# Performance work log

Measured on AMD Instinct MI355X. Metric: run time of the kernel, lower is better.

The kernel has to match this reference:

```python
import jax, jax.numpy as jnp
import numpy as np

B, N_AIM, N_DET, C = 4, 2048, 2048, 256  # inplanes=256, inter_channels=128


def _lin(x, w, b):
    # torch nn.Linear: y = x @ W^T + b, weight shape [out, in]
    return jnp.einsum('bnc,dc->bnd', x, w) + b


def setup_inputs() -> dict:
    key = jax.random.key(0)
    ks = jax.random.split(key, 16)
    s = 1.0 / np.sqrt(C)
    inp = {
        'detect': jax.random.normal(ks[0], (B, N_DET, C), jnp.float32),
        'aim': jax.random.normal(ks[1], (B, N_AIM, C), jnp.float32),
    }
    names = ['g', 'g2', 'theta', 'phi', 'W', 'Q']
    for i, nm in enumerate(names):
        inp[nm + '_w'] = jax.random.uniform(ks[2 + 2 * i], (C, C), jnp.float32, -s, s)
        inp[nm + '_b'] = jax.random.uniform(ks[3 + 2 * i], (C,), jnp.float32, -s, s)
    return inp


def reference(detect, aim, g_w, g_b, g2_w, g2_b, theta_w, theta_b, phi_w, phi_b, W_w, W_b, Q_w, Q_b):
    b, na, c = aim.shape
    nd = detect.shape[1]
    ic = c // 2  # inter_channels

    # view(B, ic, -1) on a contiguous [B, N, C] tensor -> row-major reshape to [B, ic, 2N]
    d_x = _lin(detect, g_w, g_b).reshape(b, ic, -1).transpose(0, 2, 1)      # (B, 2Nd, ic)
    a_x = _lin(aim, g2_w, g2_b).reshape(b, ic, -1).transpose(0, 2, 1)       # (B, 2Na, ic)
    theta_x = _lin(aim, theta_w, theta_b).reshape(b, ic, -1).transpose(0, 2, 1)  # (B, 2Na, ic)
    phi_x = _lin(detect, phi_w, phi_b).reshape(b, ic, -1)                   # (B, ic, 2Nd)

    f = jnp.matmul(theta_x, phi_x)                 # (B, 2Na, 2Nd)
    f_div_C = f / f.shape[-1]                      # scale by 2*Nd
    fi_div_C = jnp.swapaxes(f, 1, 2) / f.shape[-2] # (B, 2Nd, 2Na), scale by 2*Na

    non_aim = jnp.matmul(f_div_C, d_x)             # (B, 2Na, ic)
    non_aim = non_aim.transpose(0, 2, 1).reshape(b, na, c)
    non_aim = _lin(non_aim, W_w, W_b) + aim

    non_det = jnp.matmul(fi_div_C, a_x)            # (B, 2Nd, ic)
    non_det = non_det.transpose(0, 2, 1).reshape(b, nd, c)
    non_det = _lin(non_det, Q_w, Q_b) + detect

    return (non_det, non_aim)
```

## Files before the change

kernel.cpp:

```cpp
#include <hip/hip_runtime.h>


typedef __attribute__((ext_vector_type(4))) float  f32x4;
typedef __attribute__((ext_vector_type(8))) __bf16 bf16x8;
typedef __attribute__((ext_vector_type(8))) unsigned short u16x8;
typedef __attribute__((ext_vector_type(4))) unsigned short u16x4;

__device__ inline unsigned short f2bf(float f) {
    union { float f; unsigned u; } c; c.f = f;
    unsigned r = c.u + 0x7FFF + ((c.u >> 16) & 1);
    return (unsigned short)(r >> 16);
}
__device__ inline bf16x8 ldfrag(const unsigned short* p) {
    return __builtin_bit_cast(bf16x8, *(const u16x8*)p);
}

__global__ __launch_bounds__(256)
void prep_kernel(const float* __restrict__ g_w, const float* __restrict__ g2_w,
                 const float* __restrict__ th_w, const float* __restrict__ ph_w,
                 const float* __restrict__ W_w, const float* __restrict__ Q_w,
                 const float* __restrict__ aim, const float* __restrict__ detect,
                 unsigned short* __restrict__ dst)
{
    const int z = blockIdx.y;
    const float* src; size_t n4; unsigned short* o;
    if (z == 0)      { src = g_w;    n4 = 16384;  o = dst; }
    else if (z == 1) { src = g2_w;   n4 = 16384;  o = dst + 65536; }
    else if (z == 2) { src = th_w;   n4 = 16384;  o = dst + 2 * 65536; }
    else if (z == 3) { src = ph_w;   n4 = 16384;  o = dst + 3 * 65536; }
    else if (z == 4) { src = W_w;    n4 = 16384;  o = dst + 4 * 65536; }
    else if (z == 5) { src = Q_w;    n4 = 16384;  o = dst + 5 * 65536; }
    else if (z == 6) { src = aim;    n4 = 524288; o = dst + 6 * 65536; }
    else             { src = detect; n4 = 524288; o = dst + 6 * 65536 + 2097152; }
    const size_t stride = (size_t)gridDim.x * 256;
    for (size_t i = blockIdx.x * 256 + threadIdx.x; i < n4; i += stride) {
        float4 v = ((const float4*)src)[i];
        u16x4 p; p[0]=f2bf(v.x); p[1]=f2bf(v.y); p[2]=f2bf(v.z); p[3]=f2bf(v.w);
        ((u16x4*)o)[i] = p;
    }
}

__global__ __launch_bounds__(256)
void lin4_kernel(const unsigned short* __restrict__ Abf, const unsigned short* __restrict__ Dbf,
                 const unsigned short* __restrict__ Wb,
                 const float* __restrict__ b_g, const float* __restrict__ b_g2,
                 const float* __restrict__ b_th, const float* __restrict__ b_ph,
                 unsigned short* __restrict__ T,  unsigned short* __restrict__ Ga,
                 unsigned short* __restrict__ P,  unsigned short* __restrict__ Gd)
{
    const int z = blockIdx.z, set = blockIdx.x;
    const unsigned short* A = z ? Dbf : Abf;
    const int wslot = z ? (set ? 0 : 3) : (set ? 1 : 2);
    const unsigned short* Wm = Wb + (size_t)wslot * 65536;
    const float* Bv = z ? (set ? b_g : b_ph) : (set ? b_g2 : b_th);
    unsigned short* O = z ? (set ? Gd : P) : (set ? Ga : T);
    const int m0 = blockIdx.y * 64;

    __shared__ unsigned short As[64][40];
    __shared__ unsigned short Bs[256][40];

    const int tid = threadIdx.x, lane = tid & 63, w = tid >> 6;
    const int wr = w >> 1, wc = w & 1, q = lane >> 4, ln = lane & 15;

    f32x4 acc[2][8] = {};

    for (int k0 = 0; k0 < 256; k0 += 32) {
        {
            int row = tid >> 2, c8 = tid & 3;
            *(u16x8*)&As[row][c8 * 8] = *(const u16x8*)(A + (size_t)(m0 + row) * 256 + k0 + c8 * 8);
        }
        #pragma unroll
        for (int i = 0; i < 4; ++i) {
            int c = tid + i * 256, row = c >> 2, c8 = c & 3;
            *(u16x8*)&Bs[row][c8 * 8] = *(const u16x8*)(Wm + (size_t)row * 256 + k0 + c8 * 8);
        }
        __syncthreads();
        bf16x8 af[2], bb[8];
        #pragma unroll
        for (int i = 0; i < 2; ++i) af[i] = ldfrag(&As[wr * 32 + i * 16 + ln][q * 8]);
        #pragma unroll
        for (int j = 0; j < 8; ++j) bb[j] = ldfrag(&Bs[wc * 128 + j * 16 + ln][q * 8]);
        #pragma unroll
        for (int i = 0; i < 2; ++i)
            #pragma unroll
            for (int j = 0; j < 8; ++j)
                acc[i][j] = __builtin_amdgcn_mfma_f32_16x16x32_bf16(af[i], bb[j], acc[i][j], 0, 0, 0);
        __syncthreads();
    }

    #pragma unroll
    for (int i = 0; i < 2; ++i)
        #pragma unroll
        for (int j = 0; j < 8; ++j) {
            int n = wc * 128 + j * 16 + ln;
            float bias = Bv[n];
            #pragma unroll
            for (int r = 0; r < 4; ++r) {
                int m = m0 + wr * 32 + i * 16 + q * 4 + r;
                O[(size_t)m * 256 + n] = f2bf(acc[i][j][r] + bias);
            }
        }
}

__global__ __launch_bounds__(256)
void s_part_kernel(const unsigned short* __restrict__ Gd, const unsigned short* __restrict__ P,
                   const unsigned short* __restrict__ Ga, const unsigned short* __restrict__ T,
                   float* __restrict__ Spart)
{
    const int bz = blockIdx.x;
    const int which = bz >> 7, rem = bz & 127, batch = rem >> 5, chunk = rem & 31;
    const unsigned short* A = (which ? Ga : Gd) + (size_t)batch * 524288;
    const unsigned short* B = (which ? T  : P ) + (size_t)batch * 524288;
    float* out = Spart + ((size_t)(which * 4 + batch) * 32 + chunk) * 16384;
    const int kbeg = chunk * 128;

    __shared__ unsigned short As[128][72], Bs[128][72];
    const int tid = threadIdx.x, lane = tid & 63, w = tid >> 6;
    const int wr = w >> 1, wc = w & 1, q = lane >> 4, ln = lane & 15;

    f32x4 acc[4][4] = {};

    for (int kk = 0; kk < 2; ++kk) {
        const int k0 = kbeg + kk * 64;
        #pragma unroll
        for (int i = 0; i < 4; ++i) {
            int c = tid + i * 256, row = c >> 3, c8 = c & 7;
            *(u16x8*)&As[row][c8 * 8] = *(const u16x8*)(A + (size_t)row * 4096 + k0 + c8 * 8);
            *(u16x8*)&Bs[row][c8 * 8] = *(const u16x8*)(B + (size_t)row * 4096 + k0 + c8 * 8);
        }
        __syncthreads();
        #pragma unroll
        for (int ks = 0; ks < 2; ++ks) {
            bf16x8 af[4], bb[4];
            #pragma unroll
            for (int i = 0; i < 4; ++i) af[i] = ldfrag(&As[wr * 64 + i * 16 + ln][ks * 32 + q * 8]);
            #pragma unroll
            for (int j = 0; j < 4; ++j) bb[j] = ldfrag(&Bs[wc * 64 + j * 16 + ln][ks * 32 + q * 8]);
            #pragma unroll
            for (int i = 0; i < 4; ++i)
                #pragma unroll
                for (int j = 0; j < 4; ++j)
                    acc[i][j] = __builtin_amdgcn_mfma_f32_16x16x32_bf16(af[i], bb[j], acc[i][j], 0, 0, 0);
        }
        __syncthreads();
    }

    #pragma unroll
    for (int i = 0; i < 4; ++i)
        #pragma unroll
        for (int j = 0; j < 4; ++j)
            #pragma unroll
            for (int r = 0; r < 4; ++r) {
                int m = wr * 64 + i * 16 + q * 4 + r, n = wc * 64 + j * 16 + ln;
                out[m * 128 + n] = acc[i][j][r];
            }
}

__global__ __launch_bounds__(256)
void sred_kernel(const float* __restrict__ Spart, float* __restrict__ S)
{
    const int idx = blockIdx.x * 256 + threadIdx.x;
    const int c = idx >> 14, e = idx & 16383;
    float s = 0.f;
    #pragma unroll
    for (int k = 0; k < 32; ++k) s += Spart[((size_t)(c * 32 + k) << 14) + e];
    S[idx] = s;
}

__global__ __launch_bounds__(256)
void nand_kernel(const float* __restrict__ S,
                 const unsigned short* __restrict__ T, const unsigned short* __restrict__ P,
                 unsigned short* __restrict__ NA, unsigned short* __restrict__ ND)
{
    const int which = blockIdx.z >> 2, batch = blockIdx.z & 3;
    const float* Sm = S + (size_t)(which * 4 + batch) * 16384;
    const unsigned short* Bsrc = (which ? P : T) + (size_t)batch * 524288;
    unsigned short* O = (which ? ND : NA) + (size_t)batch * 524288;
    const int j0 = blockIdx.x * 64;

    __shared__ unsigned short As[128][136];
    __shared__ unsigned short Bs[64][136];

    const int tid = threadIdx.x, lane = tid & 63, w = tid >> 6;
    const int wr = w >> 1, wc = w & 1, q = lane >> 4, ln = lane & 15;

    #pragma unroll
    for (int i = 0; i < 16; ++i) {
        int c = tid + i * 256, row = c >> 5, c4 = c & 31;
        float4 v = *((const float4*)(Sm + (size_t)row * 128) + c4);
        u16x4 p; p[0]=f2bf(v.x); p[1]=f2bf(v.y); p[2]=f2bf(v.z); p[3]=f2bf(v.w);
        *(u16x4*)&As[row][c4 * 4] = p;
    }
    #pragma unroll
    for (int i = 0; i < 4; ++i) {
        int c = tid + i * 256, k = c >> 3, jj0 = (c & 7) * 8;
        u16x8 v = *(const u16x8*)(Bsrc + (size_t)k * 4096 + j0 + jj0);
        #pragma unroll
        for (int jj = 0; jj < 8; ++jj) Bs[jj0 + jj][k] = v[jj];
    }
    __syncthreads();

    f32x4 acc[4][2] = {};
    #pragma unroll
    for (int ks = 0; ks < 4; ++ks) {
        bf16x8 af[4], bb[2];
        #pragma unroll
        for (int i = 0; i < 4; ++i) af[i] = ldfrag(&As[wr * 64 + i * 16 + ln][ks * 32 + q * 8]);
        #pragma unroll
        for (int j = 0; j < 2; ++j) bb[j] = ldfrag(&Bs[wc * 32 + j * 16 + ln][ks * 32 + q * 8]);
        #pragma unroll
        for (int i = 0; i < 4; ++i)
            #pragma unroll
            for (int j = 0; j < 2; ++j)
                acc[i][j] = __builtin_amdgcn_mfma_f32_16x16x32_bf16(af[i], bb[j], acc[i][j], 0, 0, 0);
    }

    #pragma unroll
    for (int i = 0; i < 4; ++i)
        #pragma unroll
        for (int j = 0; j < 2; ++j)
            #pragma unroll
            for (int r = 0; r < 4; ++r) {
                int m = wr * 64 + i * 16 + q * 4 + r;
                int jj = j0 + wc * 32 + j * 16 + ln;
                O[(size_t)m * 4096 + jj] = f2bf(acc[i][j][r] * (1.0f / 4096.0f));
            }
}

__global__ __launch_bounds__(256)
void final_kernel(const unsigned short* __restrict__ NA, const unsigned short* __restrict__ ND,
                  const unsigned short* __restrict__ Wb,
                  const float* __restrict__ W_b, const float* __restrict__ Q_b,
                  const float* __restrict__ aim, const float* __restrict__ detect,
                  float* __restrict__ out_aim, float* __restrict__ out_det)
{
    const int z = blockIdx.z;
    const unsigned short* A = z ? ND : NA;
    const unsigned short* Wm = Wb + (size_t)(z ? 5 : 4) * 65536;
    const float* Bv = z ? Q_b : W_b;
    const float* R  = z ? detect : aim;
    float* O = z ? out_det : out_aim;
    const int m0 = blockIdx.y * 64, n0 = blockIdx.x * 128;

    __shared__ unsigned short As[64][40], Bs[128][40];
    const int tid = threadIdx.x, lane = tid & 63, w = tid >> 6;
    const int wr = w >> 1, wc = w & 1, q = lane >> 4, ln = lane & 15;

    f32x4 acc[2][4] = {};

    for (int k0 = 0; k0 < 256; k0 += 32) {
        {
            int row = tid >> 2, c8 = tid & 3;
            *(u16x8*)&As[row][c8 * 8] = *(const u16x8*)(A + (size_t)(m0 + row) * 256 + k0 + c8 * 8);
        }
        #pragma unroll
        for (int i = 0; i < 2; ++i) {
            int c = tid + i * 256, row = c >> 2, c8 = c & 3;
            *(u16x8*)&Bs[row][c8 * 8] = *(const u16x8*)(Wm + (size_t)(n0 + row) * 256 + k0 + c8 * 8);
        }
        __syncthreads();
        bf16x8 af[2], bb[4];
        #pragma unroll
        for (int i = 0; i < 2; ++i) af[i] = ldfrag(&As[wr * 32 + i * 16 + ln][q * 8]);
        #pragma unroll
        for (int j = 0; j < 4; ++j) bb[j] = ldfrag(&Bs[wc * 64 + j * 16 + ln][q * 8]);
        #pragma unroll
        for (int i = 0; i < 2; ++i)
            #pragma unroll
            for (int j = 0; j < 4; ++j)
                acc[i][j] = __builtin_amdgcn_mfma_f32_16x16x32_bf16(af[i], bb[j], acc[i][j], 0, 0, 0);
        __syncthreads();
    }

    #pragma unroll
    for (int i = 0; i < 2; ++i)
        #pragma unroll
        for (int j = 0; j < 4; ++j) {
            int n = n0 + wc * 64 + j * 16 + ln;
            float bias = Bv[n];
            #pragma unroll
            for (int r = 0; r < 4; ++r) {
                int m = m0 + wr * 32 + i * 16 + q * 4 + r;
                O[(size_t)m * 256 + n] = acc[i][j][r] + bias + R[(size_t)m * 256 + n];
            }
        }
}

extern "C" void kernel_launch(void* const* d_in, const int* in_sizes, int n_in,
                              void* d_out, int out_size, void* d_ws, size_t ws_size,
                              hipStream_t stream)
{
    const float* detect = (const float*)d_in[0];
    const float* aim    = (const float*)d_in[1];
    const float* g_w  = (const float*)d_in[2];  const float* g_b  = (const float*)d_in[3];
    const float* g2_w = (const float*)d_in[4];  const float* g2_b = (const float*)d_in[5];
    const float* th_w = (const float*)d_in[6];  const float* th_b = (const float*)d_in[7];
    const float* ph_w = (const float*)d_in[8];  const float* ph_b = (const float*)d_in[9];
    const float* W_w  = (const float*)d_in[10]; const float* W_b  = (const float*)d_in[11];
    const float* Q_w  = (const float*)d_in[12]; const float* Q_b  = (const float*)d_in[13];

    const size_t TOT = 8192L * 256;

    unsigned short* ws16 = (unsigned short*)d_ws;
    unsigned short* Wbf = ws16;
    unsigned short* Abf = Wbf + 6 * 65536;
    unsigned short* Dbf = Abf + TOT;
    unsigned short* T   = Dbf + TOT;
    unsigned short* P   = T  + TOT;
    unsigned short* Gd  = P  + TOT;
    unsigned short* Ga  = Gd + TOT;
    unsigned short* NA  = Ga + TOT;
    unsigned short* ND  = NA + TOT;
    float* S     = (float*)(ND + TOT);
    float* Spart = S + 2 * 4 * 16384;

    float* out_det = (float*)d_out;
    float* out_aim = out_det + TOT;

    prep_kernel<<<dim3(256, 8), 256, 0, stream>>>(
        g_w, g2_w, th_w, ph_w, W_w, Q_w, aim, detect, Wbf);
    lin4_kernel<<<dim3(2, 128, 2), 256, 0, stream>>>(
        Abf, Dbf, Wbf, g_b, g2_b, th_b, ph_b, T, Ga, P, Gd);
    s_part_kernel<<<dim3(256), 256, 0, stream>>>(Gd, P, Ga, T, Spart);
    sred_kernel<<<dim3(512), 256, 0, stream>>>(Spart, S);
    nand_kernel<<<dim3(64, 1, 8), 256, 0, stream>>>(S, T, P, NA, ND);
    final_kernel<<<dim3(2, 128, 2), 256, 0, stream>>>(
        NA, ND, Wbf, W_b, Q_b, aim, detect, out_aim, out_det);
}
```

Before: 138.2 us.

## Reassociate output projection before attention product and merge into mid kernel

Reorders the matmul chain so the W/Q output projections are applied to theta/phi features first (T·W, P·Q), computed in the same launch as the split-K S partials, and the small S matrix then multiplies the projected features directly in a combine kernel that adds bias and residual. This removes one full-size intermediate (NA/ND) round trip and one kernel launch. The S scaling and bf16 rounding move into the reduction kernel. The combine kernel uses a strided gather with a transposed LDS store for the B operand, which may add bank conflicts, and the changed rounding order alters numerics slightly.

```diff
diff --git a/kernel.cpp b/kernel.cpp
--- a/kernel.cpp
+++ b/kernel.cpp
@@ -103,185 +103,192 @@
 }
 
 __global__ __launch_bounds__(256)
-void s_part_kernel(const unsigned short* __restrict__ Gd, const unsigned short* __restrict__ P,
-                   const unsigned short* __restrict__ Ga, const unsigned short* __restrict__ T,
-                   float* __restrict__ Spart)
-{
-    const int bz = blockIdx.x;
-    const int which = bz >> 7, rem = bz & 127, batch = rem >> 5, chunk = rem & 31;
-    const unsigned short* A = (which ? Ga : Gd) + (size_t)batch * 524288;
-    const unsigned short* B = (which ? T  : P ) + (size_t)batch * 524288;
-    float* out = Spart + ((size_t)(which * 4 + batch) * 32 + chunk) * 16384;
-    const int kbeg = chunk * 128;
-
-    __shared__ unsigned short As[128][72], Bs[128][72];
+void mid_kernel(const unsigned short* __restrict__ Gd, const unsigned short* __restrict__ P,
+                const unsigned short* __restrict__ Ga, const unsigned short* __restrict__ T,
+                const unsigned short* __restrict__ Wb,
+                float* __restrict__ Spart,
+                unsigned short* __restrict__ TW, unsigned short* __restrict__ PQ)
+{
+    __shared__ unsigned short lds[18432];
+
     const int tid = threadIdx.x, lane = tid & 63, w = tid >> 6;
     const int wr = w >> 1, wc = w & 1, q = lane >> 4, ln = lane & 15;
 
-    f32x4 acc[4][4] = {};
-
-    for (int kk = 0; kk < 2; ++kk) {
-        const int k0 = kbeg + kk * 64;
-        #pragma unroll
-        for (int i = 0; i < 4; ++i) {
-            int c = tid + i * 256, row = c >> 3, c8 = c & 7;
-            *(u16x8*)&As[row][c8 * 8] = *(const u16x8*)(A + (size_t)row * 4096 + k0 + c8 * 8);
-            *(u16x8*)&Bs[row][c8 * 8] = *(const u16x8*)(B + (size_t)row * 4096 + k0 + c8 * 8);
-        }
-        __syncthreads();
-        #pragma unroll
-        for (int ks = 0; ks < 2; ++ks) {
-            bf16x8 af[4], bb[4];
-            #pragma unroll
-            for (int i = 0; i < 4; ++i) af[i] = ldfrag(&As[wr * 64 + i * 16 + ln][ks * 32 + q * 8]);
-            #pragma unroll
-            for (int j = 0; j < 4; ++j) bb[j] = ldfrag(&Bs[wc * 64 + j * 16 + ln][ks * 32 + q * 8]);
-            #pragma unroll
-            for (int i = 0; i < 4; ++i)
-                #pragma unroll
-                for (int j = 0; j < 4; ++j)
+    if (blockIdx.x < 256) {
+        const int bz = blockIdx.x;
+        const int which = bz >> 7, rem = bz & 127, batch = rem >> 5, chunk = rem & 31;
+        const unsigned short* A = (which ? Ga : Gd) + (size_t)batch * 524288;
+        const unsigned short* B = (which ? T  : P ) + (size_t)batch * 524288;
+        float* out = Spart + ((size_t)(which * 4 + batch) * 32 + chunk) * 16384;
+        const int kbeg = chunk * 128;
+
+        unsigned short (*As)[72] = (unsigned short (*)[72])lds;
+        unsigned short (*Bs)[72] = (unsigned short (*)[72])(lds + 9216);
+
+        f32x4 acc[4][4] = {};
+
+        for (int kk = 0; kk < 2; ++kk) {
+            const int k0 = kbeg + kk * 64;
+            #pragma unroll
+            for (int i = 0; i < 4; ++i) {
+                int c = tid + i * 256, row = c >> 3, c8 = c & 7;
+                *(u16x8*)&As[row][c8 * 8] = *(const u16x8*)(A + (size_t)row * 4096 + k0 + c8 * 8);
+                *(u16x8*)&Bs[row][c8 * 8] = *(const u16x8*)(B + (size_t)row * 4096 + k0 + c8 * 8);
+            }
+            __syncthreads();
+            #pragma unroll
+            for (int ks = 0; ks < 2; ++ks) {
+                bf16x8 af[4], bb[4];
+                #pragma unroll
+                for (int i = 0; i < 4; ++i) af[i] = ldfrag(&As[wr * 64 + i * 16 + ln][ks * 32 + q * 8]);
+                #pragma unroll
+                for (int j = 0; j < 4; ++j) bb[j] = ldfrag(&Bs[wc * 64 + j * 16 + ln][ks * 32 + q * 8]);
+                #pragma unroll
+                for (int i = 0; i < 4; ++i)
+                    #pragma unroll
+                    for (int j = 0; j < 4; ++j)
+                        acc[i][j] = __builtin_amdgcn_mfma_f32_16x16x32_bf16(af[i], bb[j], acc[i][j], 0, 0, 0);
+            }
+            __syncthreads();
+        }
+
+        #pragma unroll
+        for (int i = 0; i < 4; ++i)
+            #pragma unroll
+            for (int j = 0; j < 4; ++j)
+                #pragma unroll
+                for (int r = 0; r < 4; ++r) {
+                    int m = wr * 64 + i * 16 + q * 4 + r, n = wc * 64 + j * 16 + ln;
+                    out[m * 128 + n] = acc[i][j][r];
+                }
+    } else {
+        const int bx = blockIdx.x - 256;
+        const int side = bx >> 7, mtile = bx & 127;
+        const unsigned short* A = side ? P : T;
+        const unsigned short* Wm = Wb + (size_t)(4 + side) * 65536;
+        unsigned short* O = side ? PQ : TW;
+        const int m0 = mtile * 64;
+
+        unsigned short (*As)[40] = (unsigned short (*)[40])lds;
+        unsigned short (*Bs)[40] = (unsigned short (*)[40])(lds + 64 * 40);
+
+        f32x4 acc[2][8] = {};
+
+        for (int k0 = 0; k0 < 256; k0 += 32) {
+            {
+                int row = tid >> 2, c8 = tid & 3;
+                *(u16x8*)&As[row][c8 * 8] = *(const u16x8*)(A + (size_t)(m0 + row) * 256 + k0 + c8 * 8);
+            }
+            #pragma unroll
+            for (int i = 0; i < 4; ++i) {
+                int c = tid + i * 256, row = c >> 2, c8 = c & 3;
+                *(u16x8*)&Bs[row][c8 * 8] = *(const u16x8*)(Wm + (size_t)row * 256 + k0 + c8 * 8);
+            }
+            __syncthreads();
+            bf16x8 af[2], bb[8];
+            #pragma unroll
+            for (int i = 0; i < 2; ++i) af[i] = ldfrag(&As[wr * 32 + i * 16 + ln][q * 8]);
+            #pragma unroll
+            for (int j = 0; j < 8; ++j) bb[j] = ldfrag(&Bs[wc * 128 + j * 16 + ln][q * 8]);
+            #pragma unroll
+            for (int i = 0; i < 2; ++i)
+                #pragma unroll
+                for (int j = 0; j < 8; ++j)
                     acc[i][j] = __builtin_amdgcn_mfma_f32_16x16x32_bf16(af[i], bb[j], acc[i][j], 0, 0, 0);
-        }
-        __syncthreads();
+            __syncthreads();
+        }
+
+        #pragma unroll
+        for (int i = 0; i < 2; ++i)
+            #pragma unroll
+            for (int j = 0; j < 8; ++j) {
+                int n = wc * 128 + j * 16 + ln;
+                #pragma unroll
+                for (int r = 0; r < 4; ++r) {
+                    int m = m0 + wr * 32 + i * 16 + q * 4 + r;
+                    O[(size_t)m * 256 + n] = f2bf(acc[i][j][r]);
+                }
+            }
     }
-
-    #pragma unroll
-    for (int i = 0; i < 4; ++i)
-        #pragma unroll
-        for (int j = 0; j < 4; ++j)
-            #pragma unroll
-            for (int r = 0; r < 4; ++r) {
-                int m = wr * 64 + i * 16 + q * 4 + r, n = wc * 64 + j * 16 + ln;
-                out[m * 128 + n] = acc[i][j][r];
-            }
-}
-
-__global__ __launch_bounds__(256)
-void sred_kernel(const float* __restrict__ Spart, float* __restrict__ S)
+}
+
+__global__ __launch_bounds__(256)
+void sred_kernel(const float* __restrict__ Spart, unsigned short* __restrict__ Sbf)
 {
     const int idx = blockIdx.x * 256 + threadIdx.x;
     const int c = idx >> 14, e = idx & 16383;
     float s = 0.f;
     #pragma unroll
     for (int k = 0; k < 32; ++k) s += Spart[((size_t)(c * 32 + k) << 14) + e];
-    S[idx] = s;
-}
-
-__global__ __launch_bounds__(256)
-void nand_kernel(const float* __restrict__ S,
-                 const unsigned short* __restrict__ T, const unsigned short* __restrict__ P,
-                 unsigned short* __restrict__ NA, unsigned short* __restrict__ ND)
+    Sbf[idx] = f2bf(s * (1.0f / 4096.0f));
+}
+
+__global__ __launch_bounds__(256)
+void combine_kernel(const unsigned short* __restrict__ Sbf,
+                    const unsigned short* __restrict__ TW, const unsigned short* __restrict__ PQ,
+                    const float* __restrict__ W_b, const float* __restrict__ Q_b,
+                    const float* __restrict__ aim, const float* __restrict__ detect,
+                    float* __restrict__ out_aim, float* __restrict__ out_det)
 {
     const int which = blockIdx.z >> 2, batch = blockIdx.z & 3;
-    const float* Sm = S + (size_t)(which * 4 + batch) * 16384;
-    const unsigned short* Bsrc = (which ? P : T) + (size_t)batch * 524288;
-    unsigned short* O = (which ? ND : NA) + (size_t)batch * 524288;
-    const int j0 = blockIdx.x * 64;
-
-    __shared__ unsigned short As[128][136];
-    __shared__ unsigned short Bs[64][136];
+    const int qq = blockIdx.y, d0 = blockIdx.x * 128;
+    const unsigned short* Sm = Sbf + (size_t)(which * 4 + batch) * 16384;
+    const unsigned short* Bsrc = (which ? PQ : TW) + (size_t)batch * 524288;
+    const float* Bv = which ? Q_b : W_b;
+    const float* R  = (which ? detect : aim) + (size_t)batch * 524288;
+    float* O = (which ? out_det : out_aim) + (size_t)batch * 524288;
+
+    __shared__ unsigned short As[128][72];
+    __shared__ unsigned short Bs[128][72];
 
     const int tid = threadIdx.x, lane = tid & 63, w = tid >> 6;
     const int wr = w >> 1, wc = w & 1, q = lane >> 4, ln = lane & 15;
 
-    #pragma unroll
-    for (int i = 0; i < 16; ++i) {
-        int c = tid + i * 256, row = c >> 5, c4 = c & 31;
-        float4 v = *((const float4*)(Sm + (size_t)row * 128) + c4);
-        u16x4 p; p[0]=f2bf(v.x); p[1]=f2bf(v.y); p[2]=f2bf(v.z); p[3]=f2bf(v.w);
-        *(u16x4*)&As[row][c4 * 4] = p;
-    }
-    #pragma unroll
-    for (int i = 0; i < 4; ++i) {
-        int c = tid + i * 256, k = c >> 3, jj0 = (c & 7) * 8;
-        u16x8 v = *(const u16x8*)(Bsrc + (size_t)k * 4096 + j0 + jj0);
-        #pragma unroll
-        for (int jj = 0; jj < 8; ++jj) Bs[jj0 + jj][k] = v[jj];
-    }
-    __syncthreads();
-
-    f32x4 acc[4][2] = {};
-    #pragma unroll
-    for (int ks = 0; ks < 4; ++ks) {
-        bf16x8 af[4], bb[2];
-        #pragma unroll
-        for (int i = 0; i < 4; ++i) af[i] = ldfrag(&As[wr * 64 + i * 16 + ln][ks * 32 + q * 8]);
-        #pragma unroll
-        for (int j = 0; j < 2; ++j) bb[j] = ldfrag(&Bs[wc * 32 + j * 16 + ln][ks * 32 + q * 8]);
-        #pragma unroll
-        for (int i = 0; i < 4; ++i)
-            #pragma unroll
-            for (int j = 0; j < 2; ++j)
-                acc[i][j] = __builtin_amdgcn_mfma_f32_16x16x32_bf16(af[i], bb[j], acc[i][j], 0, 0, 0);
+    f32x4 acc[4][4] = {};
+
+    for (int kk = 0; kk < 2; ++kk) {
+        const int k0 = kk * 64;
+        #pragma unroll
+        for (int i = 0; i < 4; ++i) {
+            int c = tid + i * 256, row = c >> 3, c8 = c & 7;
+            *(u16x8*)&As[row][c8 * 8] = *(const u16x8*)(Sm + (size_t)row * 128 + k0 + c8 * 8);
+        }
+        #pragma unroll
+        for (int i = 0; i < 4; ++i) {
+            int c = tid + i * 256, krow = c >> 4, dc = (c & 15) * 8;
+            int gr = 16 * (k0 + krow) + qq;
+            u16x8 v = *(const u16x8*)(Bsrc + (size_t)gr * 256 + d0 + dc);
+            #pragma unroll
+            for (int jj = 0; jj < 8; ++jj) Bs[dc + jj][krow] = v[jj];
+        }
+        __syncthreads();
+        #pragma unroll
+        for (int ks = 0; ks < 2; ++ks) {
+            bf16x8 af[4], bb[4];
+            #pragma unroll
+            for (int i = 0; i < 4; ++i) af[i] = ldfrag(&As[wr * 64 + i * 16 + ln][ks * 32 + q * 8]);
+            #pragma unroll
+            for (int j = 0; j < 4; ++j) bb[j] = ldfrag(&Bs[wc * 64 + j * 16 + ln][ks * 32 + q * 8]);
+            #pragma unroll
+            for (int i = 0; i < 4; ++i)
+                #pragma unroll
+                for (int j = 0; j < 4; ++j)
+                    acc[i][j] = __builtin_amdgcn_mfma_f32_16x16x32_bf16(af[i], bb[j], acc[i][j], 0, 0, 0);
+        }
+        __syncthreads();
     }
 
     #pragma unroll
     for (int i = 0; i < 4; ++i)
         #pragma unroll
-        for (int j = 0; j < 2; ++j)
+        for (int j = 0; j < 4; ++j) {
+            int d = d0 + wc * 64 + j * 16 + ln;
+            float bias = Bv[d];
             #pragma unroll
             for (int r = 0; r < 4; ++r) {
-                int m = wr * 64 + i * 16 + q * 4 + r;
-                int jj = j0 + wc * 32 + j * 16 + ln;
-                O[(size_t)m * 4096 + jj] = f2bf(acc[i][j][r] * (1.0f / 4096.0f));
-            }
-}
-
-__global__ __launch_bounds__(256)
-void final_kernel(const unsigned short* __restrict__ NA, const unsigned short* __restrict__ ND,
-                  const unsigned short* __restrict__ Wb,
-                  const float* __restrict__ W_b, const float* __restrict__ Q_b,
-                  const float* __restrict__ aim, const float* __restrict__ detect,
-                  float* __restrict__ out_aim, float* __restrict__ out_det)
-{
-    const int z = blockIdx.z;
-    const unsigned short* A = z ? ND : NA;
-    const unsigned short* Wm = Wb + (size_t)(z ? 5 : 4) * 65536;
-    const float* Bv = z ? Q_b : W_b;
-    const float* R  = z ? detect : aim;
-    float* O = z ? out_det : out_aim;
-    const int m0 = blockIdx.y * 64, n0 = blockIdx.x * 128;
-
-    __shared__ unsigned short As[64][40], Bs[128][40];
-    const int tid = threadIdx.x, lane = tid & 63, w = tid >> 6;
-    const int wr = w >> 1, wc = w & 1, q = lane >> 4, ln = lane & 15;
-
-    f32x4 acc[2][4] = {};
-
-    for (int k0 = 0; k0 < 256; k0 += 32) {
-        {
-            int row = tid >> 2, c8 = tid & 3;
-            *(u16x8*)&As[row][c8 * 8] = *(const u16x8*)(A + (size_t)(m0 + row) * 256 + k0 + c8 * 8);
-        }
-        #pragma unroll
-        for (int i = 0; i < 2; ++i) {
-            int c = tid + i * 256, row = c >> 2, c8 = c & 3;
-            *(u16x8*)&Bs[row][c8 * 8] = *(const u16x8*)(Wm + (size_t)(n0 + row) * 256 + k0 + c8 * 8);
-        }
-        __syncthreads();
-        bf16x8 af[2], bb[4];
-        #pragma unroll
-        for (int i = 0; i < 2; ++i) af[i] = ldfrag(&As[wr * 32 + i * 16 + ln][q * 8]);
-        #pragma unroll
-        for (int j = 0; j < 4; ++j) bb[j] = ldfrag(&Bs[wc * 64 + j * 16 + ln][q * 8]);
-        #pragma unroll
-        for (int i = 0; i < 2; ++i)
-            #pragma unroll
-            for (int j = 0; j < 4; ++j)
-                acc[i][j] = __builtin_amdgcn_mfma_f32_16x16x32_bf16(af[i], bb[j], acc[i][j], 0, 0, 0);
-        __syncthreads();
-    }
-
-    #pragma unroll
-    for (int i = 0; i < 2; ++i)
-        #pragma unroll
-        for (int j = 0; j < 4; ++j) {
-            int n = n0 + wc * 64 + j * 16 + ln;
-            float bias = Bv[n];
-            #pragma unroll
-            for (int r = 0; r < 4; ++r) {
-                int m = m0 + wr * 32 + i * 16 + q * 4 + r;
-                O[(size_t)m * 256 + n] = acc[i][j][r] + bias + R[(size_t)m * 256 + n];
+                int iS = wr * 64 + i * 16 + q * 4 + r;
+                size_t off = (size_t)(16 * iS + qq) * 256 + d;
+                O[off] = acc[i][j][r] + bias + R[off];
             }
         }
 }
@@ -309,10 +316,10 @@
     unsigned short* P   = T  + TOT;
     unsigned short* Gd  = P  + TOT;
     unsigned short* Ga  = Gd + TOT;
-    unsigned short* NA  = Ga + TOT;
-    unsigned short* ND  = NA + TOT;
-    float* S     = (float*)(ND + TOT);
-    float* Spart = S + 2 * 4 * 16384;
+    unsigned short* TW  = Ga + TOT;
+    unsigned short* PQ  = TW + TOT;
+    unsigned short* Sbf = PQ + TOT;
+    float* Spart = (float*)(Sbf + 131072);
 
     float* out_det = (float*)d_out;
     float* out_aim = out_det + TOT;
@@ -321,9 +328,8 @@
         g_w, g2_w, th_w, ph_w, W_w, Q_w, aim, detect, Wbf);
     lin4_kernel<<<dim3(2, 128, 2), 256, 0, stream>>>(
         Abf, Dbf, Wbf, g_b, g2_b, th_b, ph_b, T, Ga, P, Gd);
-    s_part_kernel<<<dim3(256), 256, 0, stream>>>(Gd, P, Ga, T, Spart);
-    sred_kernel<<<dim3(512), 256, 0, stream>>>(Spart, S);
-    nand_kernel<<<dim3(64, 1, 8), 256, 0, stream>>>(S, T, P, NA, ND);
-    final_kernel<<<dim3(2, 128, 2), 256, 0, stream>>>(
-        NA, ND, Wbf, W_b, Q_b, aim, detect, out_aim, out_det);
-}
+    mid_kernel<<<dim3(512), 256, 0, stream>>>(Gd, P, Ga, T, Wbf, Spart, TW, PQ);
+    sred_kernel<<<dim3(512), 256, 0, stream>>>(Spart, Sbf);
+    combine_kernel<<<dim3(2, 16, 8), 256, 0, stream>>>(
+        Sbf, TW, PQ, W_b, Q_b, aim, detect, out_aim, out_det);
+}
```

Result: slower. 152.8 us (+10.6%).
